# Performance work log

Measured on AMD Instinct MI355X. Metric: run time of the kernel, lower is better.

Reference implementation:

```python
import math
import jax, jax.numpy as jnp
import numpy as np

EPS_LN = 1e-5
EPS_NORM = 1e-12


def conv2d(x, w, b=None, groups=1):
    # x: (B,C,H,W), w: (O, I//groups, kh, kw)
    out = jax.lax.conv_general_dilated(
        x, w, window_strides=(1, 1), padding='SAME',
        dimension_numbers=('NCHW', 'OIHW', 'NCHW'),
        feature_group_count=groups)
    if b is not None:
        out = out + b[None, :, None, None]
    return out


def layernorm2d(x, w, b):
    # LayerNorm over channel dim of (B,C,H,W)
    mu = x.mean(axis=1, keepdims=True)
    var = ((x - mu) ** 2).mean(axis=1, keepdims=True)
    xn = (x - mu) / jnp.sqrt(var + EPS_LN)
    return xn * w[None, :, None, None] + b[None, :, None, None]


def l2norm(x):
    n = jnp.sqrt((x * x).sum(axis=-1, keepdims=True))
    return x / jnp.maximum(n, EPS_NORM)


def mha(s, Wi, bi, Wo, bo, num_heads):
    # torch nn.MultiheadAttention (batch_first) self-attention
    B, S, C = s.shape
    Dh = C // num_heads
    qkv = s @ Wi.T + bi                      # (B,S,3C)
    q, k, v = jnp.split(qkv, 3, axis=-1)
    hd = lambda t: t.reshape(B, S, num_heads, Dh).transpose(0, 2, 1, 3)
    q, k, v = hd(q), hd(k), hd(v)            # (B,H,S,Dh)
    attn = jax.nn.softmax(jnp.einsum('bhqd,bhkd->bhqk', q, k) / math.sqrt(Dh), axis=-1)
    o = jnp.einsum('bhqk,bhkd->bhqd', attn, v).transpose(0, 2, 1, 3).reshape(B, S, C)
    return o @ Wo.T + bo


def frfn(x, pconv_w, lin1_w, lin1_b, dw_w, dw_b, lin2_w, lin2_b):
    b, c, h, w = x.shape
    dc = c // 4
    x1 = conv2d(x[:, :dc], pconv_w)                       # partial conv, no bias
    x = jnp.concatenate([x1, x[:, dc:]], axis=1)
    xt = x.transpose(0, 2, 3, 1).reshape(b, h * w, c)
    y = jax.nn.gelu(xt @ lin1_w.T + lin1_b, approximate=False)  # (b,hw,2*hid)
    y1, y2 = jnp.split(y, 2, axis=-1)
    hid = lin1_w.shape[0] // 2
    y1 = y1.reshape(b, h, w, hid).transpose(0, 3, 1, 2)
    y1 = jax.nn.gelu(conv2d(y1, dw_w, dw_b, groups=hid), approximate=False)
    y1 = y1.transpose(0, 2, 3, 1).reshape(b, h * w, hid)
    out = (y1 * y2) @ lin2_w.T + lin2_b
    return out.reshape(b, h, w, c).transpose(0, 3, 1, 2)


def setup_inputs() -> dict:
    key = jax.random.key(0)
    ks = jax.random.split(key, 10)
    B, C, H, W = 16, 256, 64, 64
    HID = 2 * C  # FRFN hidden = embed_dim*2
    DC = C // 4
    w = lambda k, shape: (jax.random.normal(k, shape, dtype=jnp.float32) * 0.02)
    return {
        'x': jax.random.normal(ks[0], (B, C, H, W), dtype=jnp.float32),
        'slot_scale': jnp.asarray(C ** -0.5, dtype=jnp.float32),
        'norm1_w': jnp.ones((C,), jnp.float32), 'norm1_b': jnp.zeros((C,), jnp.float32),
        'in_proj_w': w(ks[1], (3 * C, C)), 'in_proj_b': jnp.zeros((3 * C,), jnp.float32),
        'out_proj_w': w(ks[2], (C, C)), 'out_proj_b': jnp.zeros((C,), jnp.float32),
        'norm2_w': jnp.ones((C,), jnp.float32), 'norm2_b': jnp.zeros((C,), jnp.float32),
        'pconv_w': w(ks[3], (DC, DC, 3, 3)),
        'lin1_w': w(ks[4], (2 * HID, C)), 'lin1_b': jnp.zeros((2 * HID,), jnp.float32),
        'dw_w': w(ks[5], (HID, 1, 3, 3)), 'dw_b': jnp.zeros((HID,), jnp.float32),
        'lin2_w': w(ks[6], (C, HID)), 'lin2_b': jnp.zeros((C,), jnp.float32),
    }


def reference(x, slot_scale, norm1_w, norm1_b, in_proj_w, in_proj_b,
              out_proj_w, out_proj_b, norm2_w, norm2_b,
              pconv_w, lin1_w, lin1_b, dw_w, dw_b, lin2_w, lin2_b):
    NUM_HEADS, POOL = 8, 8
    b, c, h, w = x.shape
    copy = x
    # ada_avgpool slot init: 8x8 exact block means (h,w divisible by pool)
    pooled = x.reshape(b, c, POOL, h // POOL, POOL, w // POOL).mean(axis=(3, 5))  # (b,c,8,8)
    init_slots = pooled.transpose(0, 2, 3, 1).reshape(b, POOL * POOL, c)          # (b,S,c)

    shortcut = x
    xn = layernorm2d(x, norm1_w, norm1_b)
    xf = xn.transpose(0, 2, 3, 1).reshape(b, h * w, c)                            # (b,N,c)
    logits = slot_scale * jnp.einsum('bsc,bnc->bsn', l2norm(init_slots), l2norm(xf))
    slots = jnp.einsum('bsn,bnc->bsc', jax.nn.softmax(logits, axis=-1), xf)
    slots = mha(slots, in_proj_w, in_proj_b, out_proj_w, out_proj_b, NUM_HEADS)
    out = jnp.einsum('bns,bsc->bnc', jax.nn.softmax(logits.transpose(0, 2, 1), axis=-1), slots)
    out = out.transpose(0, 2, 1).reshape(b, c, h, w)

    x = shortcut + out
    x = x + frfn(layernorm2d(x, norm2_w, norm2_b),
                 pconv_w, lin1_w, lin1_b, dw_w, dw_b, lin2_w, lin2_b)
    return (x, copy - x)
```

## Files before the change

### kernel.cpp

```cpp
#include <hip/hip_runtime.h>
#include <hip/hip_bf16.h>
#include <stdint.h>
#include <math.h>

#define BB 16
#define CC 256
#define HH 64
#define WW 64
#define NN 4096
#define SS 64
#define NHEAD 8
#define DH 32
#define HID 512
#define DC 64

typedef float    f32x4  __attribute__((ext_vector_type(4)));
typedef uint16_t u16x8  __attribute__((ext_vector_type(8)));
typedef uint16_t u16x4  __attribute__((ext_vector_type(4)));
typedef uint16_t u16x2  __attribute__((ext_vector_type(2)));

__device__ __forceinline__ float gelu_fast(float x){
  float z = x * (1.5957691216057308f + 0.07135481627613705f * x * x);
  float e = __expf(z);
  float r = __builtin_amdgcn_rcpf(e + 1.0f);
  return x * e * r;
}
__device__ __forceinline__ uint16_t f2b(float f){
  union { float f; uint32_t u; } v; v.f = f;
  uint32_t r = v.u + 0x7fffu + ((v.u >> 16) & 1u);
  return (uint16_t)(r >> 16);
}
__device__ __forceinline__ float b2f(uint16_t h){
  union { uint32_t u; float f; } v; v.u = ((uint32_t)h) << 16;
  return v.f;
}

__device__ __forceinline__ float waveSum(float v){
#pragma unroll
  for (int m = 32; m >= 1; m >>= 1) v += __shfl_xor(v, m, 64);
  return v;
}
__device__ __forceinline__ float blockSum256(float v, float* s4){
  v = waveSum(v);
  __syncthreads();
  if ((threadIdx.x & 63) == 0) s4[threadIdx.x >> 6] = v;
  __syncthreads();
  return s4[0] + s4[1] + s4[2] + s4[3];
}

__device__ __forceinline__ void g2l16(const void* g, void* l){
  __builtin_amdgcn_global_load_lds((const __attribute__((address_space(1))) uint32_t*)g,
                                   (__attribute__((address_space(3))) uint32_t*)l, 16, 0, 0);
}

__device__ __forceinline__ int swz8(int row, int kp){ return (kp ^ (row & 7)) << 3; }

__device__ __forceinline__ void mfma_bf16(f32x4& d, u16x8 a, u16x8 b){
  asm volatile("v_mfma_f32_16x16x32_bf16 %0, %1, %2, %0" : "+v"(d) : "v"(a), "v"(b));
}

template<int SWA, int SWB>
__device__ __forceinline__ void mma_core(const uint16_t* lA, int lda, const uint16_t* lB, int ldb,
                                         f32x4 (&acc)[4][4], int wrow, int wcol, int lane){
  const int rb = lane & 15, ub = lane >> 4;
#pragma unroll
  for (int ks = 0; ks < 2; ks++){
    const int u = ks * 4 + ub;
    u16x8 af[4], bf[4];
#pragma unroll
    for (int m = 0; m < 4; m++){
      int r = wrow + m * 16 + rb;
      int e = SWA ? ((u ^ (r & 7)) << 3) : (u << 3);
      af[m] = *(const u16x8*)&lA[r * lda + e];
    }
#pragma unroll
    for (int n = 0; n < 4; n++){
      int r = wcol + n * 16 + rb;
      int e = SWB ? ((u ^ (r & 7)) << 3) : (u << 3);
      bf[n] = *(const u16x8*)&lB[r * ldb + e];
    }
#pragma unroll
    for (int m = 0; m < 4; m++)
#pragma unroll
      for (int n = 0; n < 4; n++)
        mfma_bf16(acc[m][n], af[m], bf[n]);
  }
}

__global__ __launch_bounds__(256) void k_t2b(const float* __restrict__ in, uint16_t* __restrict__ out){
  __shared__ float tile[64][33];
  int b = blockIdx.z;
  int n0 = blockIdx.x * 32;
  int c0 = blockIdx.y * 64;
  int tx = threadIdx.x, ty = threadIdx.y;
  const float* src = in + (size_t)b * CC * NN;
#pragma unroll
  for (int i = 0; i < 64; i += 8)
    tile[ty + i][tx] = src[(size_t)(c0 + ty + i) * NN + n0 + tx];
  __syncthreads();
  uint16_t* dst = out + (size_t)b * NN * CC;
#pragma unroll
  for (int i = 0; i < 32; i += 8){
    int r = ty + i;
    u16x2 o; o[0] = f2b(tile[tx * 2][r]); o[1] = f2b(tile[tx * 2 + 1][r]);
    *(u16x2*)&dst[(size_t)(n0 + r) * CC + c0 + tx * 2] = o;
  }
}

__global__ __launch_bounds__(256) void k_pool(const uint16_t* __restrict__ xhwcb, uint16_t* __restrict__ slotsNb){
  int bs = blockIdx.x; int b = bs >> 6, s = bs & 63;
  int sy = (s >> 3) * 8, sx = (s & 7) * 8;
  int t = threadIdx.x;
  int c4 = t & 63, pg = t >> 6;
  const uint16_t* base = xhwcb + (size_t)b * NN * CC;
  float a0 = 0.f, a1 = 0.f, a2 = 0.f, a3 = 0.f;
#pragma unroll
  for (int i = 0; i < 16; i++){
    int p = pg * 16 + i; int py = p >> 3, px = p & 7;
    u16x4 v = *(const u16x4*)&base[(size_t)((sy + py) * WW + sx + px) * CC + c4 * 4];
    a0 += b2f(v[0]); a1 += b2f(v[1]); a2 += b2f(v[2]); a3 += b2f(v[3]);
  }
  __shared__ float sm[4][64][4];
  sm[pg][c4][0] = a0; sm[pg][c4][1] = a1; sm[pg][c4][2] = a2; sm[pg][c4][3] = a3;
  __syncthreads();
  if (t < 64){
    float v0 = (sm[0][t][0] + sm[1][t][0] + sm[2][t][0] + sm[3][t][0]) * (1.0f / 64.0f);
    float v1 = (sm[0][t][1] + sm[1][t][1] + sm[2][t][1] + sm[3][t][1]) * (1.0f / 64.0f);
    float v2 = (sm[0][t][2] + sm[1][t][2] + sm[2][t][2] + sm[3][t][2]) * (1.0f / 64.0f);
    float v3 = (sm[0][t][3] + sm[1][t][3] + sm[2][t][3] + sm[3][t][3]) * (1.0f / 64.0f);
    float ss = waveSum(v0 * v0 + v1 * v1 + v2 * v2 + v3 * v3);
    float inv = 1.0f / fmaxf(sqrtf(ss), 1e-12f);
    u16x4 o; o[0] = f2b(v0 * inv); o[1] = f2b(v1 * inv); o[2] = f2b(v2 * inv); o[3] = f2b(v3 * inv);
    *(u16x4*)&slotsNb[(size_t)bs * CC + t * 4] = o;
  }
}

__global__ __launch_bounds__(256) void k_ln_w(const uint16_t* __restrict__ xa, const uint16_t* __restrict__ xb,
                                              const float* __restrict__ w, const float* __restrict__ b,
                                              uint16_t* __restrict__ xoutb, float* __restrict__ rn,
                                              uint16_t* __restrict__ xn2p){
  int row = blockIdx.x * 4 + (threadIdx.x >> 6);
  int lane = threadIdx.x & 63;
  u16x4 va = *(const u16x4*)&xa[(size_t)row * CC + lane * 4];
  float v0 = b2f(va[0]), v1 = b2f(va[1]), v2 = b2f(va[2]), v3 = b2f(va[3]);
  if (xb){
    u16x4 vb = *(const u16x4*)&xb[(size_t)row * CC + lane * 4];
    v0 += b2f(vb[0]); v1 += b2f(vb[1]); v2 += b2f(vb[2]); v3 += b2f(vb[3]);
  }
  float mu = waveSum(v0 + v1 + v2 + v3) * (1.0f / CC);
  float d0 = v0 - mu, d1 = v1 - mu, d2 = v2 - mu, d3 = v3 - mu;
  float var = waveSum(d0 * d0 + d1 * d1 + d2 * d2 + d3 * d3) * (1.0f / CC);
  float inv = rsqrtf(var + 1e-5f);
  float4 wv = *(const float4*)&w[lane * 4];
  float4 bv = *(const float4*)&b[lane * 4];
  float x0 = d0 * inv * wv.x + bv.x;
  float x1 = d1 * inv * wv.y + bv.y;
  float x2 = d2 * inv * wv.z + bv.z;
  float x3 = d3 * inv * wv.w + bv.w;
  u16x4 o; o[0] = f2b(x0); o[1] = f2b(x1); o[2] = f2b(x2); o[3] = f2b(x3);
  *(u16x4*)&xoutb[(size_t)row * CC + lane * 4] = o;
  if (xn2p && lane < 16){
    int bb = row >> 12, n = row & 4095, y = n >> 6, x = n & 63;
    *(u16x4*)&xn2p[(((size_t)(bb * 66 + y + 1)) * 66 + x + 1) * 64 + lane * 4] = o;
  }
  if (rn){
    float ss = waveSum(x0 * x0 + x1 * x1 + x2 * x2 + x3 * x3);
    if (lane == 0) rn[row] = 1.0f / fmaxf(sqrtf(ss), 1e-12f);
  }
}

__global__ __launch_bounds__(256) void k_zb(uint16_t* __restrict__ xn2p){
  int i = blockIdx.x * 256 + threadIdx.x;
  if (i >= 16 * 260 * 16) return;
  int c4 = i & 15; int rest = i >> 4;
  int j = rest % 260; int b = rest / 260;
  int py, px;
  if (j < 66){ py = 0; px = j; }
  else if (j < 132){ py = 65; px = j - 66; }
  else if (j < 196){ py = j - 132 + 1; px = 0; }
  else { py = j - 196 + 1; px = 65; }
  u16x4 z; z[0] = 0; z[1] = 0; z[2] = 0; z[3] = 0;
  *(u16x4*)&xn2p[(((size_t)(b * 66 + py)) * 66 + px) * 64 + c4 * 4] = z;
}

__global__ __launch_bounds__(256) void k_cvtw(const float* __restrict__ wi, const float* __restrict__ wo,
                                              const float* __restrict__ w1, const float* __restrict__ w2,
                                              const float* __restrict__ pw, const float* __restrict__ dww,
                                              uint16_t* __restrict__ wib, uint16_t* __restrict__ wob,
                                              uint16_t* __restrict__ w1b, uint16_t* __restrict__ w2b,
                                              uint16_t* __restrict__ wp2, float* __restrict__ dwwT){
  int i = blockIdx.x * 256 + threadIdx.x;
  if (i < 163840){
    const float* src; uint16_t* dst; int off;
    if (i < 49152){ src = wi; dst = wib; off = i; }
    else if (i < 65536){ src = wo; dst = wob; off = i - 49152; }
    else if (i < 131072){ src = w1; dst = w1b; off = i - 65536; }
    else { src = w2; dst = w2b; off = i - 131072; }
    float4 v = ((const float4*)src)[off];
    u16x4 o;
    o[0] = f2b(v.x); o[1] = f2b(v.y); o[2] = f2b(v.z); o[3] = f2b(v.w);
    *(u16x4*)&dst[(size_t)off * 4] = o;
  } else if (i < 200704){
    int j = i - 163840;
    if (j < 64 * 576){
      int co = j / 576, r = j % 576, tap = r >> 6, ci = r & 63;
      wp2[j] = f2b(pw[(size_t)co * 576 + ci * 9 + tap]);
    }
  } else {
    int j = i - 200704;
    if (j < 9 * HID){
      int tap = j / HID, ch = j % HID;
      dwwT[j] = dww[(size_t)ch * 9 + tap];
    }
  }
}

__global__ __launch_bounds__(256) void k_txT(const uint16_t* __restrict__ xnb, uint16_t* __restrict__ xnTb){
  __shared__ uint16_t tile[64 * 66];
  int b = blockIdx.z;
  int n0 = blockIdx.x * 64, c0 = blockIdx.y * 64;
  int t = threadIdx.x;
#pragma unroll
  for (int i = 0; i < 16; i++){
    int idx = i * 256 + t;
    int nr = idx >> 6, c = idx & 63;
    tile[c * 66 + nr] = xnb[((size_t)b * NN + n0 + nr) * CC + c0 + c];
  }
  __syncthreads();
#pragma unroll
  for (int i = 0; i < 16; i++){
    int idx = i * 256 + t;
    int cr = idx >> 6, n = idx & 63;
    xnTb[((size_t)b * CC + c0 + cr) * NN + n0 + n] = tile[cr * 66 + n];
  }
}

__global__ __launch_bounds__(256) void k_logits_mfma(const uint16_t* __restrict__ slotsNb,
                                                     const uint16_t* __restrict__ xnb,
                                                     const float* __restrict__ rn,
                                                     const float* __restrict__ scale_p,
                                                     uint16_t* __restrict__ E){
  __shared__ uint16_t smem[20480];
  __shared__ float rnS[256];
  uint16_t* lA = smem;
  uint16_t* lB = smem + 64 * 64;
  int t = threadIdx.x, lane = t & 63, w = t >> 6;
  int b = blockIdx.y, n0 = blockIdx.x * 256;
  rnS[t] = rn[b * NN + n0 + t];
  f32x4 acc[4][4];
#pragma unroll
  for (int m = 0; m < 4; m++)
#pragma unroll
    for (int n = 0; n < 4; n++) acc[m][n] = (f32x4){0.f, 0.f, 0.f, 0.f};
  for (int kc = 0; kc < 4; kc++){
#pragma unroll
    for (int i = 0; i < 2; i++){
      int idx = i * 256 + t, row = idx >> 3, kp = idx & 7;
      *(u16x8*)&lA[row * 64 + swz8(row, kp)] = *(const u16x8*)&slotsNb[(size_t)(b * 64 + row) * 256 + kc * 64 + kp * 8];
    }
#pragma unroll
    for (int i = 0; i < 8; i++){
      int idx = i * 256 + t, row = idx >> 3, kp = idx & 7;
      *(u16x8*)&lB[row * 64 + swz8(row, kp)] = *(const u16x8*)&xnb[((size_t)b * NN + n0 + row) * 256 + kc * 64 + kp * 8];
    }
    __syncthreads();
    mma_core<1, 1>(lA, 64, lB, 64, acc, 0, w * 64, lane);
    __syncthreads();
  }
  float scale = scale_p[0];
  int rb4 = (lane >> 4) * 4, cb = lane & 15;
#pragma unroll
  for (int m = 0; m < 4; m++)
#pragma unroll
    for (int n = 0; n < 4; n++)
#pragma unroll
      for (int j = 0; j < 4; j++){
        int s = m * 16 + rb4 + j, nl = w * 64 + n * 16 + cb;
        smem[s * 264 + nl] = f2b(__expf(acc[m][n][j] * scale * rnS[nl]));
      }
  __syncthreads();
#pragma unroll
  for (int i = 0; i < 8; i++){
    int idx = i * 256 + t, row = idx >> 5, cseg = idx & 31;
    *(u16x8*)&E[((size_t)b * 64 + row) * NN + n0 + cseg * 8] = *(const u16x8*)&smem[row * 264 + cseg * 8];
  }
}

__global__ __launch_bounds__(256) void k_z1(const uint16_t* __restrict__ E, float* __restrict__ invz1){
  int bs = blockIdx.x, t = threadIdx.x;
  u16x8 v0 = *(const u16x8*)&E[(size_t)bs * NN + t * 16];
  u16x8 v1 = *(const u16x8*)&E[(size_t)bs * NN + t * 16 + 8];
  float s = 0.f;
#pragma unroll
  for (int i = 0; i < 8; i++) s += b2f(v0[i]) + b2f(v1[i]);
  __shared__ float s4[4];
  float z = blockSum256(s, s4);
  if (t == 0) invz1[bs] = 1.0f / z;
}

__global__ __launch_bounds__(256) void k_slots_mfma(const uint16_t* __restrict__ E,
                                                    const uint16_t* __restrict__ xnTb,
                                                    float* __restrict__ part){
  __shared__ uint16_t lA[64 * 64];
  __shared__ uint16_t lB[256 * 64];
  int t = threadIdx.x, lane = t & 63, w = t >> 6;
  int ks = blockIdx.x, b = blockIdx.y;
  f32x4 acc[4][4];
#pragma unroll
  for (int m = 0; m < 4; m++)
#pragma unroll
    for (int n = 0; n < 4; n++) acc[m][n] = (f32x4){0.f, 0.f, 0.f, 0.f};
  for (int kc = 0; kc < 8; kc++){
    int n0 = ks * 512 + kc * 64;
#pragma unroll
    for (int i = 0; i < 2; i++){
      int q = (w * 2 + i) * 64 + lane;
      int row = q >> 3, kpe = swz8(row, q & 7);
      g2l16(&E[((size_t)b * 64 + row) * NN + n0 + kpe], &lA[(w * 2 + i) * 512]);
    }
#pragma unroll
    for (int i = 0; i < 8; i++){
      int q = (w * 8 + i) * 64 + lane;
      int row = q >> 3, kpe = swz8(row, q & 7);
      g2l16(&xnTb[((size_t)b * CC + row) * NN + n0 + kpe], &lB[(w * 8 + i) * 512]);
    }
    __syncthreads();
    mma_core<1, 1>(lA, 64, lB, 64, acc, 0, w * 64, lane);
    __syncthreads();
  }
  int rb4 = (lane >> 4) * 4, cb = lane & 15;
#pragma unroll
  for (int m = 0; m < 4; m++)
#pragma unroll
    for (int n = 0; n < 4; n++)
#pragma unroll
      for (int j = 0; j < 4; j++){
        int s = m * 16 + rb4 + j, c = w * 64 + n * 16 + cb;
        part[(((size_t)b * 8 + ks) * 64 + s) * 256 + c] = acc[m][n][j];
      }
}

__global__ __launch_bounds__(256) void k_fold(const float* __restrict__ part, const float* __restrict__ invz1,
                                              uint16_t* __restrict__ slotsb){
  int i = blockIdx.x * 256 + threadIdx.x;
  int row = i >> 6, c4 = i & 63;
  int b = row >> 6, s = row & 63;
  float4 a = {0.f, 0.f, 0.f, 0.f};
#pragma unroll
  for (int p = 0; p < 8; p++){
    float4 v = *(const float4*)&part[(((size_t)b * 8 + p) * 64 + s) * 256 + c4 * 4];
    a.x += v.x; a.y += v.y; a.z += v.z; a.w += v.w;
  }
  float iz = invz1[row];
  u16x4 o; o[0] = f2b(a.x * iz); o[1] = f2b(a.y * iz); o[2] = f2b(a.z * iz); o[3] = f2b(a.w * iz);
  *(u16x4*)&slotsb[(size_t)row * 256 + c4 * 4] = o;
}

__global__ __launch_bounds__(256) void k_gemm_qkv(const uint16_t* __restrict__ slotsb,
                                                  const uint16_t* __restrict__ wib,
                                                  const float* __restrict__ bi,
                                                  float* __restrict__ qkv){
  __shared__ uint16_t lA[128 * 64];
  __shared__ uint16_t lB[128 * 64];
  int t = threadIdx.x, lane = t & 63, w = t >> 6;
  int wrow = (w >> 1) * 64, wcol = (w & 1) * 64;
  int BR = blockIdx.x * 128, BC = blockIdx.y * 128;
  f32x4 acc[4][4];
#pragma unroll
  for (int m = 0; m < 4; m++)
#pragma unroll
    for (int n = 0; n < 4; n++) acc[m][n] = (f32x4){0.f, 0.f, 0.f, 0.f};
  for (int kc = 0; kc < 4; kc++){
#pragma unroll
    for (int i = 0; i < 4; i++){
      int idx = i * 256 + t, row = idx >> 3, kp = idx & 7;
      *(u16x8*)&lA[row * 64 + swz8(row, kp)] = *(const u16x8*)&slotsb[(size_t)(BR + row) * 256 + kc * 64 + kp * 8];
      *(u16x8*)&lB[row * 64 + swz8(row, kp)] = *(const u16x8*)&wib[(size_t)(BC + row) * 256 + kc * 64 + kp * 8];
    }
    __syncthreads();
    mma_core<1, 1>(lA, 64, lB, 64, acc, wrow, wcol, lane);
    __syncthreads();
  }
  int rb4 = (lane >> 4) * 4, cb = lane & 15;
#pragma unroll
  for (int m = 0; m < 4; m++)
#pragma unroll
    for (int n = 0; n < 4; n++){
      int c = BC + wcol + n * 16 + cb;
      float bias = bi[c];
#pragma unroll
      for (int j = 0; j < 4; j++)
        qkv[(size_t)(BR + wrow + m * 16 + rb4 + j) * 768 + c] = acc[m][n][j] + bias;
    }
}

__global__ __launch_bounds__(256) void k_attn(const float* __restrict__ qkv, uint16_t* __restrict__ aob){
  int b = blockIdx.x >> 3, h = blockIdx.x & 7;
  __shared__ float lq[64][33], lk[64][33], lv[64][33];
  __shared__ float sc[64][65];
  int t = threadIdx.x;
  for (int idx = t; idx < 64 * 32; idx += 256){
    int s = idx >> 5, d = idx & 31;
    const float* base = qkv + ((size_t)b * SS + s) * 768 + h * DH + d;
    lq[s][d] = base[0];
    lk[s][d] = base[256];
    lv[s][d] = base[512];
  }
  __syncthreads();
  const float rs = 0.17677669529663687f;
  for (int idx = t; idx < 64 * 64; idx += 256){
    int qq = idx >> 6, kk = idx & 63;
    float a = 0.f;
#pragma unroll
    for (int d = 0; d < 32; d++) a += lq[qq][d] * lk[kk][d];
    sc[qq][kk] = a * rs;
  }
  __syncthreads();
  {
    int r = t >> 2, sub = t & 3;
    float m = -1e30f;
#pragma unroll
    for (int k = sub * 16; k < sub * 16 + 16; k++) m = fmaxf(m, sc[r][k]);
    m = fmaxf(m, __shfl_xor(m, 1, 64));
    m = fmaxf(m, __shfl_xor(m, 2, 64));
    float z = 0.f;
#pragma unroll
    for (int k = sub * 16; k < sub * 16 + 16; k++){
      float e = __expf(sc[r][k] - m); sc[r][k] = e; z += e;
    }
    z += __shfl_xor(z, 1, 64);
    z += __shfl_xor(z, 2, 64);
    float iv = 1.0f / z;
#pragma unroll
    for (int k = sub * 16; k < sub * 16 + 16; k++) sc[r][k] *= iv;
  }
  __syncthreads();
  for (int idx = t; idx < 64 * 32; idx += 256){
    int qq = idx >> 5, d = idx & 31;
    float a = 0.f;
#pragma unroll
    for (int k = 0; k < 64; k++) a += sc[qq][k] * lv[k][d];
    aob[((size_t)b * SS + qq) * CC + h * DH + d] = f2b(a);
  }
}

__global__ __launch_bounds__(256) void k_gemm_oproj(const uint16_t* __restrict__ aob,
                                                    const uint16_t* __restrict__ wob,
                                                    const float* __restrict__ bo,
                                                    uint16_t* __restrict__ sl2Tb){
  __shared__ uint16_t lA[128 * 64];
  __shared__ uint16_t lB[128 * 64];
  int t = threadIdx.x, lane = t & 63, w = t >> 6;
  int wrow = (w >> 1) * 64, wcol = (w & 1) * 64;
  int BR = blockIdx.x * 128, BC = blockIdx.y * 128;
  f32x4 acc[4][4];
#pragma unroll
  for (int m = 0; m < 4; m++)
#pragma unroll
    for (int n = 0; n < 4; n++) acc[m][n] = (f32x4){0.f, 0.f, 0.f, 0.f};
  for (int kc = 0; kc < 4; kc++){
#pragma unroll
    for (int i = 0; i < 4; i++){
      int idx = i * 256 + t, row = idx >> 3, kp = idx & 7;
      *(u16x8*)&lA[row * 64 + swz8(row, kp)] = *(const u16x8*)&aob[(size_t)(BR + row) * 256 + kc * 64 + kp * 8];
      *(u16x8*)&lB[row * 64 + swz8(row, kp)] = *(const u16x8*)&wob[(size_t)(BC + row) * 256 + kc * 64 + kp * 8];
    }
    __syncthreads();
    mma_core<1, 1>(lA, 64, lB, 64, acc, wrow, wcol, lane);
    __syncthreads();
  }
  int rb4 = (lane >> 4) * 4, cb = lane & 15;
#pragma unroll
  for (int m = 0; m < 4; m++)
#pragma unroll
    for (int n = 0; n < 4; n++){
      int c = BC + wcol + n * 16 + cb;
      float bias = bo[c];
#pragma unroll
      for (int j = 0; j < 4; j++){
        int r = BR + wrow + m * 16 + rb4 + j;
        int b = r >> 6, s = r & 63;
        sl2Tb[((size_t)b * 256 + c) * 64 + s] = f2b(acc[m][n][j] + bias);
      }
    }
}

__global__ __launch_bounds__(256) void k_mix(const uint16_t* __restrict__ E, const uint16_t* __restrict__ sl2Tb,
                                             uint16_t* __restrict__ mixb){
  __shared__ uint16_t lA[128 * 72];
  __shared__ uint16_t lB[128 * 64];
  __shared__ float z2S[128];
  int t = threadIdx.x, lane = t & 63, w = t >> 6;
  int wrow = (w >> 1) * 64, wcol = (w & 1) * 64;
  int BR = blockIdx.x * 128, BC = blockIdx.y * 128, b = blockIdx.z;
#pragma unroll
  for (int i = 0; i < 4; i++){
    int idx = i * 256 + t; int s = idx >> 4, n8 = (idx & 15) * 8;
    u16x8 v = *(const u16x8*)&E[((size_t)b * 64 + s) * NN + BR + n8];
#pragma unroll
    for (int j = 0; j < 8; j++) lA[(n8 + j) * 72 + s] = v[j];
  }
#pragma unroll
  for (int i = 0; i < 4; i++){
    int idx = i * 256 + t, row = idx >> 3, kp = idx & 7;
    *(u16x8*)&lB[row * 64 + swz8(row, kp)] = *(const u16x8*)&sl2Tb[((size_t)b * 256 + BC + row) * 64 + kp * 8];
  }
  __syncthreads();
  if (t < 128){
    float s = 0.f;
#pragma unroll
    for (int k2 = 0; k2 < 64; k2++) s += b2f(lA[t * 72 + k2]);
    z2S[t] = 1.0f / s;
  }
  __syncthreads();
  f32x4 acc[4][4];
#pragma unroll
  for (int m = 0; m < 4; m++)
#pragma unroll
    for (int n = 0; n < 4; n++) acc[m][n] = (f32x4){0.f, 0.f, 0.f, 0.f};
  mma_core<0, 1>(lA, 72, lB, 64, acc, wrow, wcol, lane);
  int rb4 = (lane >> 4) * 4, cb = lane & 15;
#pragma unroll
  for (int m = 0; m < 4; m++)
#pragma unroll
    for (int n = 0; n < 4; n++)
#pragma unroll
      for (int j = 0; j < 4; j++){
        int lrow = wrow + m * 16 + rb4 + j;
        size_t gi = ((size_t)b * NN + BR + lrow) * 256 + BC + wcol + n * 16 + cb;
        mixb[gi] = f2b(acc[m][n][j] * z2S[lrow]);
      }
}

__global__ __launch_bounds__(256) void k_pconv_mfma(const uint16_t* __restrict__ xn2p,
                                                    const uint16_t* __restrict__ wp2,
                                                    uint16_t* __restrict__ pcb){
  __shared__ uint16_t lA[256 * 64];
  __shared__ uint16_t lB[64 * 64];
  int t = threadIdx.x, lane = t & 63, w = t >> 6;
  int wrow = w * 64;
  int BR = blockIdx.x * 256;
  f32x4 acc[4][4];
#pragma unroll
  for (int m = 0; m < 4; m++)
#pragma unroll
    for (int n = 0; n < 4; n++) acc[m][n] = (f32x4){0.f, 0.f, 0.f, 0.f};
  for (int tap = 0; tap < 9; tap++){
    int dy = tap / 3 - 1, dx = tap % 3 - 1;
#pragma unroll
    for (int i = 0; i < 8; i++){
      int q = (w * 8 + i) * 64 + lane;
      int row = q >> 3, kpe = swz8(row, q & 7);
      int r = BR + row;
      int b = r >> 12, n = r & 4095, y = n >> 6, x = n & 63;
      size_t p = ((size_t)(b * 66 + (y + 1 + dy)) * 66 + (x + 1 + dx)) * 64 + kpe;
      g2l16(&xn2p[p], &lA[(w * 8 + i) * 512]);
    }
#pragma unroll
    for (int i = 0; i < 2; i++){
      int q = (w * 2 + i) * 64 + lane;
      int row = q >> 3, kpe = swz8(row, q & 7);
      g2l16(&wp2[(size_t)row * 576 + tap * 64 + kpe], &lB[(w * 2 + i) * 512]);
    }
    __syncthreads();
    mma_core<1, 1>(lA, 64, lB, 64, acc, wrow, 0, lane);
    __syncthreads();
  }
  int rb4 = (lane >> 4) * 4, cb = lane & 15;
#pragma unroll
  for (int m = 0; m < 4; m++)
#pragma unroll
    for (int j = 0; j < 4; j++){
      uint16_t* rp = &pcb[(size_t)(BR + wrow + m * 16 + rb4 + j) * 64 + cb];
#pragma unroll
      for (int n = 0; n < 4; n++)
        rp[n * 16] = f2b(acc[m][n][j]);
    }
}

__global__ __launch_bounds__(256) void k_lin1_mfma(const uint16_t* __restrict__ pcb,
                                                   const uint16_t* __restrict__ xn2b,
                                                   const uint16_t* __restrict__ w1b,
                                                   const float* __restrict__ b1,
                                                   uint16_t* __restrict__ Y1b, uint16_t* __restrict__ Y2b){
  __shared__ uint16_t lA[128 * 64];
  __shared__ uint16_t lB[128 * 64];
  int t = threadIdx.x, lane = t & 63, w = t >> 6;
  int wrow = (w >> 1) * 64, wcol = (w & 1) * 64;
  int bid = blockIdx.x;
  int xcd = bid & 7, i5 = bid >> 3;
  int BR = (xcd * 64 + (i5 >> 3)) * 128;
  int BC = (i5 & 7) * 128;
  f32x4 acc[4][4];
#pragma unroll
  for (int m = 0; m < 4; m++)
#pragma unroll
    for (int n = 0; n < 4; n++) acc[m][n] = (f32x4){0.f, 0.f, 0.f, 0.f};
  for (int kc = 0; kc < 4; kc++){
#pragma unroll
    for (int i = 0; i < 4; i++){
      int q = (w * 4 + i) * 64 + lane;
      int row = q >> 3, kpe = swz8(row, q & 7);
      size_t gr = (size_t)(BR + row);
      const uint16_t* src = (kc == 0) ? &pcb[gr * 64 + kpe] : &xn2b[gr * 256 + kc * 64 + kpe];
      g2l16(src, &lA[(w * 4 + i) * 512]);
      g2l16(&w1b[(size_t)(BC + row) * 256 + kc * 64 + kpe], &lB[(w * 4 + i) * 512]);
    }
    __syncthreads();
    mma_core<1, 1>(lA, 64, lB, 64, acc, wrow, wcol, lane);
    __syncthreads();
  }
  int rb4 = (lane >> 4) * 4, cb = lane & 15;
  float bias[4];
#pragma unroll
  for (int n = 0; n < 4; n++) bias[n] = b1[BC + wcol + n * 16 + cb];
  uint16_t* dst = (BC < HID) ? (Y1b + BC + wcol + cb) : (Y2b + (BC - HID) + wcol + cb);
#pragma unroll
  for (int m = 0; m < 4; m++)
#pragma unroll
    for (int j = 0; j < 4; j++){
      uint16_t* rp = dst + (size_t)(BR + wrow + m * 16 + rb4 + j) * HID;
#pragma unroll
      for (int n = 0; n < 4; n++)
        rp[n * 16] = f2b(gelu_fast(acc[m][n][j] + bias[n]));
    }
}

__global__ __launch_bounds__(256) void k_dwconv(const uint16_t* __restrict__ Y1b,
                                                const float* __restrict__ dwwT,
                                                const float* __restrict__ dwb,
                                                const uint16_t* __restrict__ Y2b,
                                                uint16_t* __restrict__ YPb){
  __shared__ uint16_t lds[3 * 18 * 136];
  int b = blockIdx.z, chunk = blockIdx.y;
  int y = blockIdx.x >> 2, seg = blockIdx.x & 3;
  int x0 = seg * 16;
  int t = threadIdx.x;
  const uint16_t* base = Y1b + (size_t)b * NN * HID + chunk * 128;
  const u16x8 z = {0, 0, 0, 0, 0, 0, 0, 0};
#pragma unroll
  for (int i = 0; i < 4; i++){
    int idx = i * 256 + t;
    if (idx < 864){
      int g8 = idx & 15, rest = idx >> 4;
      int c = rest % 18, r = rest / 18;
      int ry = y + r - 1, xx = x0 + c - 1;
      u16x8 v = z;
      if (ry >= 0 && ry < HH && xx >= 0 && xx < WW)
        v = *(const u16x8*)&base[(size_t)(ry * WW + xx) * HID + g8 * 8];
      *(u16x8*)&lds[(r * 18 + c) * 136 + g8 * 8] = v;
    }
  }
  __syncthreads();
  int px = t >> 4, g8 = t & 15;
  int cg = chunk * 128 + g8 * 8;
  int n = y * WW + x0 + px;
  u16x8 y2 = *(const u16x8*)&Y2b[((size_t)b * NN + n) * HID + cg];
  float acc[8];
  {
    float4 b0 = *(const float4*)&dwb[cg];
    float4 b1 = *(const float4*)&dwb[cg + 4];
    acc[0] = b0.x; acc[1] = b0.y; acc[2] = b0.z; acc[3] = b0.w;
    acc[4] = b1.x; acc[5] = b1.y; acc[6] = b1.z; acc[7] = b1.w;
  }
#pragma unroll
  for (int r = 0; r < 3; r++)
#pragma unroll
    for (int dx = 0; dx < 3; dx++){
      u16x8 v = *(const u16x8*)&lds[(r * 18 + px + dx) * 136 + g8 * 8];
      const float* wt = &dwwT[(r * 3 + dx) * HID + cg];
      float4 w0 = *(const float4*)wt;
      float4 w1 = *(const float4*)(wt + 4);
      acc[0] += b2f(v[0]) * w0.x; acc[1] += b2f(v[1]) * w0.y;
      acc[2] += b2f(v[2]) * w0.z; acc[3] += b2f(v[3]) * w0.w;
      acc[4] += b2f(v[4]) * w1.x; acc[5] += b2f(v[5]) * w1.y;
      acc[6] += b2f(v[6]) * w1.z; acc[7] += b2f(v[7]) * w1.w;
    }
  u16x8 o;
#pragma unroll
  for (int j = 0; j < 8; j++) o[j] = f2b(gelu_fast(acc[j]) * b2f(y2[j]));
  *(u16x8*)&YPb[((size_t)b * NN + n) * HID + cg] = o;
}

__global__ __launch_bounds__(256) void k_lin2_mfma(const uint16_t* __restrict__ YPb,
                                                   const uint16_t* __restrict__ w2b,
                                                   const float* __restrict__ b2,
                                                   uint16_t* __restrict__ deltab){
  __shared__ uint16_t lA[128 * 64];
  __shared__ uint16_t lB[128 * 64];
  int t = threadIdx.x, lane = t & 63, w = t >> 6;
  int wrow = (w >> 1) * 64, wcol = (w & 1) * 64;
  int bid = blockIdx.x;
  int xcd = bid & 7, i5 = bid >> 3;
  int BR = (xcd * 64 + (i5 >> 1)) * 128;
  int BC = (i5 & 1) * 128;
  f32x4 acc[4][4];
#pragma unroll
  for (int m = 0; m < 4; m++)
#pragma unroll
    for (int n = 0; n < 4; n++) acc[m][n] = (f32x4){0.f, 0.f, 0.f, 0.f};
  for (int kc = 0; kc < 8; kc++){
#pragma unroll
    for (int i = 0; i < 4; i++){
      int q = (w * 4 + i) * 64 + lane;
      int row = q >> 3, kpe = swz8(row, q & 7);
      g2l16(&YPb[(size_t)(BR + row) * HID + kc * 64 + kpe], &lA[(w * 4 + i) * 512]);
      g2l16(&w2b[(size_t)(BC + row) * HID + kc * 64 + kpe], &lB[(w * 4 + i) * 512]);
    }
    __syncthreads();
    mma_core<1, 1>(lA, 64, lB, 64, acc, wrow, wcol, lane);
    __syncthreads();
  }
  int rb4 = (lane >> 4) * 4, cb = lane & 15;
  float bias[4];
#pragma unroll
  for (int n = 0; n < 4; n++) bias[n] = b2[BC + wcol + n * 16 + cb];
  uint16_t* dst = deltab + BC + wcol + cb;
#pragma unroll
  for (int m = 0; m < 4; m++)
#pragma unroll
    for (int j = 0; j < 4; j++){
      uint16_t* rp = dst + (size_t)(BR + wrow + m * 16 + rb4 + j) * CC;
#pragma unroll
      for (int n = 0; n < 4; n++)
        rp[n * 16] = f2b(acc[m][n][j] + bias[n]);
    }
}

__global__ __launch_bounds__(256) void k_final2(const uint16_t* __restrict__ mixb,
                                                const uint16_t* __restrict__ deltab,
                                                const uint16_t* __restrict__ xhwcb,
                                                float* __restrict__ out){
  __shared__ float t0[64 * 68];
  __shared__ float t1[64 * 68];
  int b = blockIdx.z;
  int n0 = blockIdx.x * 64, c0 = blockIdx.y * 64;
  int t = threadIdx.x;
#pragma unroll
  for (int i = 0; i < 4; i++){
    int idx = i * 256 + t, row = idx >> 4, c4 = idx & 15;
    size_t gp = ((size_t)b * NN + n0 + row) * CC + c0 + c4 * 4;
    u16x4 m = *(const u16x4*)&mixb[gp];
    u16x4 d = *(const u16x4*)&deltab[gp];
    u16x4 xh = *(const u16x4*)&xhwcb[gp];
    f32x4 v0, v1;
#pragma unroll
    for (int j = 0; j < 4; j++){
      float v = b2f(m[j]) + b2f(d[j]);
      v0[j] = b2f(xh[j]) + v;
      v1[j] = -v;
    }
    *(f32x4*)&t0[row * 68 + c4 * 4] = v0;
    *(f32x4*)&t1[row * 68 + c4 * 4] = v1;
  }
  __syncthreads();
  int cl = t >> 2, seg = t & 3;
  float* o1 = out + (size_t)BB * CC * NN;
  size_t gbase = ((size_t)(b * CC + c0 + cl)) * NN + n0 + seg * 16;
#pragma unroll
  for (int k = 0; k < 4; k++){
    float4 a, c;
    a.x = t0[(seg * 16 + k * 4 + 0) * 68 + cl];
    a.y = t0[(seg * 16 + k * 4 + 1) * 68 + cl];
    a.z = t0[(seg * 16 + k * 4 + 2) * 68 + cl];
    a.w = t0[(seg * 16 + k * 4 + 3) * 68 + cl];
    c.x = t1[(seg * 16 + k * 4 + 0) * 68 + cl];
    c.y = t1[(seg * 16 + k * 4 + 1) * 68 + cl];
    c.z = t1[(seg * 16 + k * 4 + 2) * 68 + cl];
    c.w = t1[(seg * 16 + k * 4 + 3) * 68 + cl];
    *(float4*)&out[gbase + k * 4] = a;
    *(float4*)&o1[gbase + k * 4] = c;
  }
}

extern "C" void kernel_launch(void* const* d_in, const int* in_sizes, int n_in,
                              void* d_out, int out_size, void* d_ws, size_t ws_size,
                              hipStream_t stream){
  const float* x       = (const float*)d_in[0];
  const float* scale_p = (const float*)d_in[1];
  const float* n1w     = (const float*)d_in[2];
  const float* n1b     = (const float*)d_in[3];
  const float* wi      = (const float*)d_in[4];
  const float* bi      = (const float*)d_in[5];
  const float* wo      = (const float*)d_in[6];
  const float* bo      = (const float*)d_in[7];
  const float* n2w     = (const float*)d_in[8];
  const float* n2b     = (const float*)d_in[9];
  const float* pw      = (const float*)d_in[10];
  const float* w1      = (const float*)d_in[11];
  const float* b1      = (const float*)d_in[12];
  const float* dww     = (const float*)d_in[13];
  const float* dwb     = (const float*)d_in[14];
  const float* w2      = (const float*)d_in[15];
  const float* b2      = (const float*)d_in[16];

  float* base = (float*)d_ws;
  size_t off = 0;
  float* part = base + off; off += (size_t)BB * 8 * SS * CC;
  float* QKV  = base + off; off += (size_t)BB * SS * 3 * CC;
  float* RN   = base + off; off += (size_t)BB * NN;
  float* IZ1  = base + off; off += (size_t)BB * SS;
  float* dwwT = base + off; off += (size_t)9 * HID;
  uint16_t* slotsNb = (uint16_t*)(base + off); off += (size_t)BB * SS * CC / 2;
  uint16_t* slotsb  = (uint16_t*)(base + off); off += (size_t)BB * SS * CC / 2;
  uint16_t* aob     = (uint16_t*)(base + off); off += (size_t)BB * SS * CC / 2;
  uint16_t* sl2Tb   = (uint16_t*)(base + off); off += (size_t)BB * CC * SS / 2;
  uint16_t* xhwcb   = (uint16_t*)(base + off); off += (size_t)BB * NN * CC / 2;
  uint16_t* xnb     = (uint16_t*)(base + off); off += (size_t)BB * NN * CC / 2;
  uint16_t* xnTb    = (uint16_t*)(base + off); off += (size_t)BB * NN * CC / 2;
  uint16_t* mixb    = (uint16_t*)(base + off); off += (size_t)BB * NN * CC / 2;
  uint16_t* deltab  = (uint16_t*)(base + off); off += (size_t)BB * NN * CC / 2;
  uint16_t* E       = (uint16_t*)(base + off); off += (size_t)BB * SS * NN / 2;
  uint16_t* w1b     = (uint16_t*)(base + off); off += (size_t)(2 * HID) * CC / 2;
  uint16_t* w2b     = (uint16_t*)(base + off); off += (size_t)CC * HID / 2;
  uint16_t* wib     = (uint16_t*)(base + off); off += (size_t)(3 * CC) * CC / 2;
  uint16_t* wob     = (uint16_t*)(base + off); off += (size_t)CC * CC / 2;
  uint16_t* wp2     = (uint16_t*)(base + off); off += (size_t)64 * 576 / 2 + 16;
  uint16_t* Y1b     = (uint16_t*)(base + off); off += (size_t)BB * NN * HID / 2;
  uint16_t* Y2b     = (uint16_t*)(base + off); off += (size_t)BB * NN * HID / 2;
  uint16_t* YPb     = (uint16_t*)(base + off); off += (size_t)BB * NN * HID / 2;
  uint16_t* xn2b    = (uint16_t*)(base + off); off += (size_t)BB * NN * CC / 2;
  uint16_t* xn2p    = (uint16_t*)(base + off); off += (size_t)BB * 66 * 66 * 64 / 2;
  uint16_t* pcb     = (uint16_t*)(base + off); off += (size_t)BB * NN * 64 / 2;
  if (ws_size < off * sizeof(float)) return;
  float* OUT = (float*)d_out;

  dim3 tb2(32, 8);
  k_t2b<<<dim3(NN / 32, CC / 64, BB), tb2, 0, stream>>>(x, xhwcb);
  k_pool<<<BB * SS, 256, 0, stream>>>(xhwcb, slotsNb);
  k_ln_w<<<BB * NN / 4, 256, 0, stream>>>(xhwcb, (const uint16_t*)nullptr, n1w, n1b, xnb, RN,
                                          (uint16_t*)nullptr);
  k_cvtw<<<803, 256, 0, stream>>>(wi, wo, w1, w2, pw, dww, wib, wob, w1b, w2b, wp2, dwwT);
  k_zb<<<(16 * 260 * 16 + 255) / 256, 256, 0, stream>>>(xn2p);
  k_logits_mfma<<<dim3(NN / 256, BB), 256, 0, stream>>>(slotsNb, xnb, RN, scale_p, E);
  k_txT<<<dim3(NN / 64, CC / 64, BB), 256, 0, stream>>>(xnb, xnTb);
  k_z1<<<BB * SS, 256, 0, stream>>>(E, IZ1);
  k_slots_mfma<<<dim3(8, BB), 256, 0, stream>>>(E, xnTb, part);
  k_fold<<<(BB * SS * CC / 4) / 256, 256, 0, stream>>>(part, IZ1, slotsb);
  k_gemm_qkv<<<dim3(8, 6), 256, 0, stream>>>(slotsb, wib, bi, QKV);
  k_attn<<<BB * NHEAD, 256, 0, stream>>>(QKV, aob);
  k_gemm_oproj<<<dim3(8, 2), 256, 0, stream>>>(aob, wob, bo, sl2Tb);
  k_mix<<<dim3(NN / 128, CC / 128, BB), 256, 0, stream>>>(E, sl2Tb, mixb);
  k_ln_w<<<BB * NN / 4, 256, 0, stream>>>(xhwcb, mixb, n2w, n2b, xn2b, (float*)nullptr, xn2p);
  k_pconv_mfma<<<BB * NN / 256, 256, 0, stream>>>(xn2p, wp2, pcb);
  k_lin1_mfma<<<4096, 256, 0, stream>>>(pcb, xn2b, w1b, b1, Y1b, Y2b);
  k_dwconv<<<dim3(256, 4, BB), 256, 0, stream>>>(Y1b, dwwT, dwb, Y2b, YPb);
  k_lin2_mfma<<<1024, 256, 0, stream>>>(YPb, w2b, b2, deltab);
  k_final2<<<dim3(NN / 64, CC / 64, BB), 256, 0, stream>>>(mixb, deltab, xhwcb, OUT);
}
```

Measured before the change: 409.6 us.

## Stage pconv halo tile once in LDS and pack depthwise math into float2

The partial-conv MFMA kernel now loads the padded input rows for its 256-pixel block, plus halo, into LDS once (3328 swizzled 16-byte chunks). Each of the 9 taps then reads shifted A fragments straight from that tile, where before it re-gathered a full A tile from global memory for every tap. The aim is to cut global-to-LDS traffic roughly ninefold for that kernel, at the cost of more LDS (about 52 KB plus B) and therefore possibly lower occupancy. Separately, the depthwise conv kernel unpacks bf16 pairs with shifts and accumulates in float2 vectors, so the compiler can emit packed FMA.

Result: no change. 409.1 us (-0.1%).

```diff
diff --git a/kernel.cpp b/kernel.cpp
--- a/kernel.cpp
+++ b/kernel.cpp
@@ -15,6 +15,8 @@
 #define DC 64
 
 typedef float    f32x4  __attribute__((ext_vector_type(4)));
+typedef float    f32x2  __attribute__((ext_vector_type(2)));
+typedef uint32_t u32x4  __attribute__((ext_vector_type(4)));
 typedef uint16_t u16x8  __attribute__((ext_vector_type(8)));
 typedef uint16_t u16x4  __attribute__((ext_vector_type(4)));
 typedef uint16_t u16x2  __attribute__((ext_vector_type(2)));
@@ -33,6 +35,11 @@
 __device__ __forceinline__ float b2f(uint16_t h){
   union { uint32_t u; float f; } v; v.u = ((uint32_t)h) << 16;
   return v.f;
+}
+__device__ __forceinline__ f32x2 bpair(uint32_t u){
+  union { uint32_t u; float f; } lo, hi;
+  lo.u = u << 16; hi.u = u & 0xffff0000u;
+  return (f32x2){lo.f, hi.f};
 }
 
 __device__ __forceinline__ float waveSum(float v){
@@ -535,27 +542,34 @@
 __global__ __launch_bounds__(256) void k_pconv_mfma(const uint16_t* __restrict__ xn2p,
                                                     const uint16_t* __restrict__ wp2,
                                                     uint16_t* __restrict__ pcb){
-  __shared__ uint16_t lA[256 * 64];
+  __shared__ uint16_t lS[3328 * 8];
   __shared__ uint16_t lB[64 * 64];
   int t = threadIdx.x, lane = t & 63, w = t >> 6;
   int wrow = w * 64;
   int BR = blockIdx.x * 256;
+  int b = BR >> 12, y0 = (BR & 4095) >> 6;
+  size_t G0 = ((size_t)(b * 66 + y0) * 66) * 64;
+#pragma unroll
+  for (int i = 0; i < 13; i++){
+    int q = i * 256 + t;
+    int li = q >> 3, kp = q & 7;
+    g2l16(&xn2p[G0 + (size_t)li * 64 + ((kp ^ (li & 7)) << 3)], &lS[q * 8]);
+  }
+  const int rb = lane & 15, ub = lane >> 4;
+  int li0[4];
+#pragma unroll
+  for (int m = 0; m < 4; m++){
+    int r = wrow + m * 16 + rb;
+    li0[m] = ((r >> 6) + 1) * 66 + (r & 63) + 1;
+  }
   f32x4 acc[4][4];
 #pragma unroll
   for (int m = 0; m < 4; m++)
 #pragma unroll
     for (int n = 0; n < 4; n++) acc[m][n] = (f32x4){0.f, 0.f, 0.f, 0.f};
+#pragma unroll
   for (int tap = 0; tap < 9; tap++){
-    int dy = tap / 3 - 1, dx = tap % 3 - 1;
-#pragma unroll
-    for (int i = 0; i < 8; i++){
-      int q = (w * 8 + i) * 64 + lane;
-      int row = q >> 3, kpe = swz8(row, q & 7);
-      int r = BR + row;
-      int b = r >> 12, n = r & 4095, y = n >> 6, x = n & 63;
-      size_t p = ((size_t)(b * 66 + (y + 1 + dy)) * 66 + (x + 1 + dx)) * 64 + kpe;
-      g2l16(&xn2p[p], &lA[(w * 8 + i) * 512]);
-    }
+    const int doff = (tap / 3 - 1) * 66 + (tap % 3 - 1);
 #pragma unroll
     for (int i = 0; i < 2; i++){
       int q = (w * 2 + i) * 64 + lane;
@@ -563,7 +577,26 @@
       g2l16(&wp2[(size_t)row * 576 + tap * 64 + kpe], &lB[(w * 2 + i) * 512]);
     }
     __syncthreads();
-    mma_core<1, 1>(lA, 64, lB, 64, acc, wrow, 0, lane);
+#pragma unroll
+    for (int ks = 0; ks < 2; ks++){
+      const int u = ks * 4 + ub;
+      u16x8 af[4], bf[4];
+#pragma unroll
+      for (int m = 0; m < 4; m++){
+        int li = li0[m] + doff;
+        af[m] = *(const u16x8*)&lS[li * 64 + ((u ^ (li & 7)) << 3)];
+      }
+#pragma unroll
+      for (int n = 0; n < 4; n++){
+        int r = n * 16 + rb;
+        bf[n] = *(const u16x8*)&lB[r * 64 + ((u ^ (r & 7)) << 3)];
+      }
+#pragma unroll
+      for (int m = 0; m < 4; m++)
+#pragma unroll
+        for (int n = 0; n < 4; n++)
+          mfma_bf16(acc[m][n], af[m], bf[n]);
+    }
     __syncthreads();
   }
   int rb4 = (lane >> 4) * 4, cb = lane & 15;
@@ -655,30 +688,33 @@
   int px = t >> 4, g8 = t & 15;
   int cg = chunk * 128 + g8 * 8;
   int n = y * WW + x0 + px;
-  u16x8 y2 = *(const u16x8*)&Y2b[((size_t)b * NN + n) * HID + cg];
-  float acc[8];
+  u32x4 y2v = *(const u32x4*)&Y2b[((size_t)b * NN + n) * HID + cg];
+  f32x2 acc2[4];
   {
     float4 b0 = *(const float4*)&dwb[cg];
     float4 b1 = *(const float4*)&dwb[cg + 4];
-    acc[0] = b0.x; acc[1] = b0.y; acc[2] = b0.z; acc[3] = b0.w;
-    acc[4] = b1.x; acc[5] = b1.y; acc[6] = b1.z; acc[7] = b1.w;
+    acc2[0] = (f32x2){b0.x, b0.y}; acc2[1] = (f32x2){b0.z, b0.w};
+    acc2[2] = (f32x2){b1.x, b1.y}; acc2[3] = (f32x2){b1.z, b1.w};
   }
 #pragma unroll
   for (int r = 0; r < 3; r++)
 #pragma unroll
     for (int dx = 0; dx < 3; dx++){
-      u16x8 v = *(const u16x8*)&lds[(r * 18 + px + dx) * 136 + g8 * 8];
-      const float* wt = &dwwT[(r * 3 + dx) * HID + cg];
-      float4 w0 = *(const float4*)wt;
-      float4 w1 = *(const float4*)(wt + 4);
-      acc[0] += b2f(v[0]) * w0.x; acc[1] += b2f(v[1]) * w0.y;
-      acc[2] += b2f(v[2]) * w0.z; acc[3] += b2f(v[3]) * w0.w;
-      acc[4] += b2f(v[4]) * w1.x; acc[5] += b2f(v[5]) * w1.y;
-      acc[6] += b2f(v[6]) * w1.z; acc[7] += b2f(v[7]) * w1.w;
+      u32x4 v = *(const u32x4*)&lds[(r * 18 + px + dx) * 136 + g8 * 8];
+      const f32x2* wt = (const f32x2*)&dwwT[(r * 3 + dx) * HID + cg];
+      acc2[0] += bpair(v[0]) * wt[0];
+      acc2[1] += bpair(v[1]) * wt[1];
+      acc2[2] += bpair(v[2]) * wt[2];
+      acc2[3] += bpair(v[3]) * wt[3];
     }
   u16x8 o;
 #pragma unroll
-  for (int j = 0; j < 8; j++) o[j] = f2b(gelu_fast(acc[j]) * b2f(y2[j]));
+  for (int j = 0; j < 4; j++){
+    f32x2 yy = bpair(y2v[j]);
+    float g0 = gelu_fast(acc2[j].x) * yy.x;
+    float g1 = gelu_fast(acc2[j].y) * yy.y;
+    o[2 * j] = f2b(g0); o[2 * j + 1] = f2b(g1);
+  }
   *(u16x8*)&YPb[((size_t)b * NN + n) * HID + cg] = o;
 }
 
```
